# Kernel tuning notes

Hardware: AMD Instinct MI355X
Metric: run time of the kernel (lower is better)

Reference implementation:

```python
import jax, jax.numpy as jnp
import numpy as np


def log_g(x):
    # log of g(x) = x + 0.5 for x>=0, sigmoid(x) for x<0
    return jnp.where(x >= 0, jnp.log(jax.nn.relu(x) + 0.5), -jax.nn.softplus(-x))


def setup_inputs() -> dict:
    key = jax.random.key(0)
    k1, k2, k3 = jax.random.split(key, 3)
    bs, seq_len, d_in, H = 4, 4096, 1024, 1024
    scale = 1.0 / np.sqrt(d_in)  # keep pre-activations O(1) so exp() in log-space scan stays finite
    x = jax.random.normal(k1, (bs, seq_len, d_in), dtype=jnp.float32)
    h_0 = jnp.zeros((bs, 1, H), dtype=jnp.float32)
    Wz = jax.random.normal(k2, (H, d_in), dtype=jnp.float32) * scale
    bz = jnp.zeros((H,), dtype=jnp.float32)
    Wh = jax.random.normal(k3, (H, d_in), dtype=jnp.float32) * scale
    bh = jnp.zeros((H,), dtype=jnp.float32)
    return {"x": x, "h_0": h_0, "Wz": Wz, "bz": bz, "Wh": Wh, "bh": bh}


def reference(x, h_0, Wz, bz, Wh, bh):
    bs, seq_len, _ = x.shape
    # gate and candidate pre-activations (two GEMMs)
    k = jnp.einsum("bsd,hd->bsh", x, Wz) + bz          # [bs, S, H]
    log_coeff = -jax.nn.softplus(k)                     # log(1 - z)
    log_z = -jax.nn.softplus(-k)                        # log(z)
    log_tilde_h = log_g(jnp.einsum("bsd,hd->bsh", x, Wh) + bh)
    log_h_0 = log_g(h_0)                                # [bs, 1, H]
    log_value = jnp.concatenate([log_h_0, log_z + log_tilde_h], axis=1)  # [bs, S+1, H]
    # log-space parallel scan: h_t = (1-z_t) h_{t-1} + z_t h~_t
    a_star = jnp.pad(jnp.cumsum(log_coeff, axis=1), ((0, 0), (1, 0), (0, 0)))  # [bs, S+1, H]
    log_h0_plus_b_star = jax.lax.cumlogsumexp(log_value - a_star, axis=1)
    log_prefix = a_star + log_h0_plus_b_star
    return jnp.exp(log_prefix)[:, 1:]                   # [bs, S, H]
```

## Files before the change

### kernel.cpp

```cpp
#include <hip/hip_runtime.h>
#include <cstddef>
#include <cstdint>

#define BSZ   4
#define SEQ   4096
#define DIN   1024
#define HDIM  1024
#define MTOT  (BSZ * SEQ)
#define NELE  ((size_t)MTOT * HDIM)
#define NX    ((size_t)MTOT * DIN)
#define NW    ((size_t)HDIM * DIN)
#define NCH   128
#define CL    (SEQ / NCH)

#define X4 (NX / 4)
#define W4 (NW / 4)

#define GBM 256
#define GBN 128
#define GBK 64
#define NKT (DIN / GBK)

using bf16x8 = __attribute__((ext_vector_type(8))) __bf16;
using f32x4  = __attribute__((ext_vector_type(4))) float;

__device__ __forceinline__ float bf2f(unsigned int u16bits) {
    union { unsigned int i; float f; } v;
    v.i = u16bits << 16;
    return v.f;
}
__device__ __forceinline__ unsigned int pk2(float a, float b) {
    union { float f; unsigned int i; } ua, ub; ua.f = a; ub.f = b;
    return ((ua.i + 0x8000u) >> 16) | ((ub.i + 0x8000u) & 0xffff0000u);
}

__device__ __forceinline__ void gload16(const void* g, void* l) {
    __builtin_amdgcn_global_load_lds(
        (const __attribute__((address_space(1))) unsigned int*)g,
        (__attribute__((address_space(3))) unsigned int*)l, 16, 0, 0);
}

__global__ __launch_bounds__(256) void cvt_bf16(
    const float* __restrict__ x, const float* __restrict__ wz,
    const float* __restrict__ wh, unsigned short* __restrict__ xb,
    unsigned short* __restrict__ zb, unsigned short* __restrict__ hb)
{
    const size_t i = (size_t)blockIdx.x * 256 + threadIdx.x;
    const float4* s; uint4* d; size_t off;
    const size_t xh = X4 / 2, wh4 = W4 / 2;
    if (i < xh)            { s = (const float4*)x;  d = (uint4*)xb; off = i; }
    else if (i < xh + wh4) { s = (const float4*)wz; d = (uint4*)zb; off = i - xh; }
    else                   { s = (const float4*)wh; d = (uint4*)hb; off = i - xh - wh4; }
    const float4 v0 = s[2 * off];
    const float4 v1 = s[2 * off + 1];
    uint4 r;
    r.x = pk2(v0.x, v0.y); r.y = pk2(v0.z, v0.w);
    r.z = pk2(v1.x, v1.y); r.w = pk2(v1.z, v1.w);
    d[off] = r;
}

#define SBAR  __builtin_amdgcn_sched_barrier(0)
#define PRIO1 __builtin_amdgcn_s_setprio(1)
#define PRIO0 __builtin_amdgcn_s_setprio(0)

#define MFMA1(acc, va, vb) \
    acc = __builtin_amdgcn_mfma_f32_16x16x32_bf16(va, vb, acc, 0, 0, 0)

#define MFMA_PAIR(P, AV, S)                                                    \
    _Pragma("unroll")                                                          \
    for (int i_ = 0; i_ < 2; ++i_) {                                           \
        _Pragma("unroll")                                                      \
        for (int nt_ = 0; nt_ < 2; ++nt_) {                                    \
            MFMA1(accz[2*(P)+i_][nt_], AV[i_][0], Bz[S][nt_][0]);              \
            MFMA1(acch[2*(P)+i_][nt_], AV[i_][0], Bh[S][nt_][0]);              \
            MFMA1(accz[2*(P)+i_][nt_], AV[i_][1], Bz[S][nt_][1]);              \
            MFMA1(acch[2*(P)+i_][nt_], AV[i_][1], Bh[S][nt_][1]);              \
        }                                                                      \
    }

#define READ_A(AV, MTP, B)                                                     \
    AV[0][0] = *(const bf16x8*)((B) + aBase + (2*(MTP)+0)*2048 + k0o);         \
    AV[0][1] = *(const bf16x8*)((B) + aBase + (2*(MTP)+0)*2048 + k1o);         \
    AV[1][0] = *(const bf16x8*)((B) + aBase + (2*(MTP)+1)*2048 + k0o);         \
    AV[1][1] = *(const bf16x8*)((B) + aBase + (2*(MTP)+1)*2048 + k1o);

#define READ_B_HALF(SS, NT, B)                                                 \
    Bz[SS][NT][0] = *(const bf16x8*)((B) + zBase + (NT)*2048 + k0o);           \
    Bz[SS][NT][1] = *(const bf16x8*)((B) + zBase + (NT)*2048 + k1o);           \
    Bh[SS][NT][0] = *(const bf16x8*)((B) + hBase + (NT)*2048 + k0o);           \
    Bh[SS][NT][1] = *(const bf16x8*)((B) + hBase + (NT)*2048 + k1o);

#define STAGE8(BN, KO)                                                         \
    gload16(gA + (KO),          (BN) + ldsA);                                  \
    gload16(gA + (KO) + 16384,  (BN) + ldsA + 512);                            \
    gload16(gA + (KO) + 32768,  (BN) + ldsA + 1024);                           \
    gload16(gA + (KO) + 49152,  (BN) + ldsA + 1536);                           \
    gload16(gZ + (KO),          (BN) + ldsZ);                                  \
    gload16(gZ + (KO) + 16384,  (BN) + ldsZ + 512);                            \
    gload16(gH + (KO),          (BN) + ldsH);                                  \
    gload16(gH + (KO) + 16384,  (BN) + ldsH + 512);

#define TILE(KT, S)                                                            \
    {                                                                          \
        const int ktv = (KT);                                                  \
        const char*     bcc = (const char*)&smem[S][0];                        \
        unsigned short* bn  = &smem[(S) ^ 1][0];                               \
        const char*     bnc = (const char*)bn;                                 \
        const bool pf = (ktv + 1 < NKT);                                       \
        const size_t ko = (size_t)(ktv + 1) * 128;                             \
                                                                       \
        if (pf) { STAGE8(bn, ko) }                                             \
        READ_A(A1, 1, bcc)                                                     \
        PRIO1; MFMA_PAIR(0, A0, S) PRIO0; SBAR;                                \
                                                                       \
        READ_A(A0, 2, bcc)                                                     \
        PRIO1; MFMA_PAIR(1, A1, S) PRIO0; SBAR;                                \
                                                                       \
        READ_A(A1, 3, bcc)                                                     \
        PRIO1; MFMA_PAIR(2, A0, S) PRIO0; SBAR;                                \
                \
        if (pf) {                                                              \
            asm volatile("s_waitcnt vmcnt(0)" ::: "memory");                   \
            __builtin_amdgcn_s_barrier();                                      \
            READ_B_HALF((S) ^ 1, 0, bnc)                                       \
            READ_A(A0, 0, bnc)                                                 \
        }                                                                      \
        PRIO1; MFMA_PAIR(3, A1, S) PRIO0; SBAR;                                \
        if (pf) { READ_B_HALF((S) ^ 1, 1, bnc) }                               \
    }

__global__ __launch_bounds__(512, 2) void gemm_act_8ph(
    const unsigned short* __restrict__ xb, const unsigned short* __restrict__ zb,
    const unsigned short* __restrict__ hb, const float* __restrict__ bz,
    const float* __restrict__ bh, unsigned int* __restrict__ ab,
    float* __restrict__ carryA, float* __restrict__ carryB)
{
    __shared__ unsigned short smem[2][32768];

    const int tid  = threadIdx.x;
    const int wid  = tid >> 6;
    const int lane = tid & 63;
    const int lm   = lane & 15;
    const int q    = lane >> 4;
    const int wr   = wid >> 2;
    const int wc   = wid & 3;

    const int bid = blockIdx.x;
    const int swz = (bid & 7) * 64 + (bid >> 3);
    const int ty  = swz >> 3;
    const int tx  = swz & 7;
    const int m0  = ty * GBM;
    const int n0  = tx * GBN;

    const int l8   = lane >> 3;
    const int sl   = lane & 7;
    const int scol = 16 * (sl ^ l8);
    const char* gA = (const char*)xb + ((size_t)(m0 + wid * 32 + l8) * DIN) * 2 + scol;
    const char* gZ = (const char*)zb + ((size_t)(n0 + wid * 16 + l8) * DIN) * 2 + scol;
    const char* gH = (const char*)hb + ((size_t)(n0 + wid * 16 + l8) * DIN) * 2 + scol;
    const int ldsA = wid * 2048;
    const int ldsZ = 16384 + wid * 1024;
    const int ldsH = 24576 + wid * 1024;

    const int sw  = (lm & 7) << 4;
    const int k0o = (q * 16) ^ sw;
    const int k1o = (64 + q * 16) ^ sw;
    const int aBase = (wr * 128 + lm) * 128;
    const int zBase = 32768 + (wc * 32 + lm) * 128;
    const int hBase = 49152 + (wc * 32 + lm) * 128;

    f32x4 accz[8][2], acch[8][2];
#pragma unroll
    for (int mt = 0; mt < 8; ++mt)
#pragma unroll
        for (int nt = 0; nt < 2; ++nt) {
            accz[mt][nt] = (f32x4){0.f, 0.f, 0.f, 0.f};
            acch[mt][nt] = (f32x4){0.f, 0.f, 0.f, 0.f};
        }

    bf16x8 A0[2][2], A1[2][2];
    bf16x8 Bz[2][2][2], Bh[2][2][2];

    {
        unsigned short* b0 = &smem[0][0];
        const char*     b0c = (const char*)b0;
        STAGE8(b0, 0)
        asm volatile("s_waitcnt vmcnt(0)" ::: "memory");
        __builtin_amdgcn_s_barrier();
        READ_B_HALF(0, 0, b0c)
        READ_B_HALF(0, 1, b0c)
        READ_A(A0, 0, b0c)
    }

    for (int kt = 0; kt < NKT; kt += 2) {
        TILE(kt, 0)
        TILE(kt + 1, 1)
    }

    const int bi  = m0 >> 12;
    const int cb0 = ((m0 & 4095) >> 5) + wr * 4;

#pragma unroll
    for (int nt = 0; nt < 2; ++nt) {
        const int col = n0 + wc * 32 + nt * 16 + lm;
        const float bzv = bz[col];
        const float bhv = bh[col];
#pragma unroll
        for (int pr = 0; pr < 4; ++pr) {
            float CA = 1.f, CB = 0.f;
#pragma unroll
            for (int mi = 0; mi < 2; ++mi) {
                const int mt   = pr * 2 + mi;
                const int row0 = m0 + wr * 128 + mt * 16 + q * 4;
                float A = 1.f, B = 0.f;
#pragma unroll
                for (int r = 0; r < 4; ++r) {
                    const float kpre = accz[mt][nt][r] + bzv;
                    const float hpre = acch[mt][nt][r] + bhv;
                    const float ez   = __expf(-kpre);
                    const float zv   = 1.0f / (1.0f + ez);
                    const float avv  = ez * zv;
                    const float g    = (hpre >= 0.f) ? (hpre + 0.5f)
                                                     : (1.0f / (1.0f + __expf(-hpre)));
                    const float bv   = zv * g;
                    ab[(size_t)(row0 + r) * HDIM + col] = pk2(avv, bv);
                    A = avv * A;
                    B = fmaf(avv, B, bv);
                }
                float A2 = __shfl_xor(A, 16, 64);
                float B2 = __shfl_xor(B, 16, 64);
                B = (q & 1) ? fmaf(A, B2, B) : fmaf(A2, B, B2);
                A = A * A2;
                A2 = __shfl_xor(A, 32, 64);
                B2 = __shfl_xor(B, 32, 64);
                B = (q & 2) ? fmaf(A, B2, B) : fmaf(A2, B, B2);
                A = A * A2;
                CB = fmaf(A, CB, B);
                CA = A * CA;
            }
            if (q == 0) {
                const int cseq = cb0 + pr;
                const size_t ci = ((size_t)(cseq * BSZ + bi)) * HDIM + col;
                carryA[ci] = CA;
                carryB[ci] = CB;
            }
        }
    }
}

__global__ __launch_bounds__(256) void scan_phaseB(
    const float* __restrict__ h0, const float* __restrict__ carryA,
    const float* __restrict__ carryB, float* __restrict__ hin)
{
    const int h  = blockIdx.x * 256 + threadIdx.x;
    const int bi = blockIdx.y;
    const float v = h0[(size_t)bi * HDIM + h];
    float hr = (v >= 0.0f) ? (v + 0.5f) : (1.0f / (1.0f + __expf(-v)));
    for (int c = 0; c < NCH; ++c) {
        const size_t ci = ((size_t)c * BSZ + bi) * HDIM + h;
        hin[ci] = hr;
        hr = fmaf(carryA[ci], hr, carryB[ci]);
    }
}

__global__ __launch_bounds__(256) void scan_phaseC(
    const unsigned int* __restrict__ ab, const float* __restrict__ hin,
    float* __restrict__ out)
{
    const int c  = blockIdx.x;
    const int bi = blockIdx.y;
    const int h  = threadIdx.x * 4;
    size_t idx = ((size_t)bi * SEQ + (size_t)c * CL) * HDIM + h;
    const size_t ci = ((size_t)c * BSZ + bi) * HDIM + h;
    float4 hr = *(const float4*)&hin[ci];
#pragma unroll 4
    for (int t = 0; t < CL; ++t) {
        const uint4 v = *(const uint4*)&ab[idx];
        hr.x = fmaf(bf2f(v.x & 0xffffu), hr.x, bf2f(v.x >> 16));
        hr.y = fmaf(bf2f(v.y & 0xffffu), hr.y, bf2f(v.y >> 16));
        hr.z = fmaf(bf2f(v.z & 0xffffu), hr.z, bf2f(v.z >> 16));
        hr.w = fmaf(bf2f(v.w & 0xffffu), hr.w, bf2f(v.w >> 16));
        *(float4*)&out[idx] = hr;
        idx += HDIM;
    }
}

extern "C" void kernel_launch(void* const* d_in, const int* in_sizes, int n_in,
                              void* d_out, int out_size, void* d_ws, size_t ws_size,
                              hipStream_t stream)
{
    const float* x  = (const float*)d_in[0];
    const float* h0 = (const float*)d_in[1];
    const float* Wz = (const float*)d_in[2];
    const float* bz = (const float*)d_in[3];
    const float* Wh = (const float*)d_in[4];
    const float* bh = (const float*)d_in[5];
    float* out = (float*)d_out;

    unsigned int*   ab  = (unsigned int*)d_ws;
    unsigned short* xbf = (unsigned short*)(ab + NELE);
    unsigned short* zbf = xbf + NX;
    unsigned short* hbf = zbf + NW;
    float* carryA = (float*)(hbf + NW);
    float* carryB = carryA + (size_t)NCH * BSZ * HDIM;
    float* hin    = carryB + (size_t)NCH * BSZ * HDIM;

    const int cvtBlocks = (int)((X4 + 2 * W4) / 2 / 256);
    cvt_bf16<<<cvtBlocks, 256, 0, stream>>>(x, Wz, Wh, xbf, zbf, hbf);

    dim3 gGrid((MTOT / GBM) * (HDIM / GBN));
    gemm_act_8ph<<<gGrid, 512, 0, stream>>>(xbf, zbf, hbf, bz, bh, ab, carryA, carryB);

    dim3 bGrid(HDIM / 256, BSZ);
    scan_phaseB<<<bGrid, 256, 0, stream>>>(h0, carryA, carryB, hin);

    dim3 cGrid(NCH, BSZ);
    scan_phaseC<<<cGrid, 256, 0, stream>>>(ab, hin, out);
}
```

Baseline: 240.1 us.

## Deepen GEMM LDS pipeline to four stages with half-size K tiles

The fused dual GEMM now uses a K tile of 32 instead of 64, spread over a four-slot LDS ring with prefetch distance two, replacing the double buffer. The LDS swizzle and fragment addressing are reworked for 64-byte rows, and the wait on outstanding loads is relaxed to vmcnt(4) so one stage can stay in flight. The goal is to hide global-to-LDS latency better behind the MFMAs, at the cost of twice as many barriers per K pass. Separately, the sequential carry scan in phase B batches eight carry loads ahead of the dependent FMA chain.

```diff
diff --git a/kernel.cpp b/kernel.cpp
--- a/kernel.cpp
+++ b/kernel.cpp
@@ -18,8 +18,8 @@
 
 #define GBM 256
 #define GBN 128
-#define GBK 64
-#define NKT (DIN / GBK)
+#define GBK 32
+#define NKT2 (DIN / GBK)
 
 using bf16x8 = __attribute__((ext_vector_type(8))) __bf16;
 using f32x4  = __attribute__((ext_vector_type(4))) float;
@@ -66,67 +66,55 @@
 #define MFMA1(acc, va, vb) \
     acc = __builtin_amdgcn_mfma_f32_16x16x32_bf16(va, vb, acc, 0, 0, 0)
 
-#define MFMA_PAIR(P, AV, S)                                                    \
+#define MFMA_PH(PH, AV, S)                                                     \
     _Pragma("unroll")                                                          \
-    for (int i_ = 0; i_ < 2; ++i_) {                                           \
+    for (int j_ = 0; j_ < 4; ++j_) {                                           \
         _Pragma("unroll")                                                      \
         for (int nt_ = 0; nt_ < 2; ++nt_) {                                    \
-            MFMA1(accz[2*(P)+i_][nt_], AV[i_][0], Bz[S][nt_][0]);              \
-            MFMA1(acch[2*(P)+i_][nt_], AV[i_][0], Bh[S][nt_][0]);              \
-            MFMA1(accz[2*(P)+i_][nt_], AV[i_][1], Bz[S][nt_][1]);              \
-            MFMA1(acch[2*(P)+i_][nt_], AV[i_][1], Bh[S][nt_][1]);              \
+            MFMA1(accz[4*(PH)+j_][nt_], AV[j_], Bz[S][nt_]);                   \
+            MFMA1(acch[4*(PH)+j_][nt_], AV[j_], Bh[S][nt_]);                   \
         }                                                                      \
     }
 
-#define READ_A(AV, MTP, B)                                                     \
-    AV[0][0] = *(const bf16x8*)((B) + aBase + (2*(MTP)+0)*2048 + k0o);         \
-    AV[0][1] = *(const bf16x8*)((B) + aBase + (2*(MTP)+0)*2048 + k1o);         \
-    AV[1][0] = *(const bf16x8*)((B) + aBase + (2*(MTP)+1)*2048 + k0o);         \
-    AV[1][1] = *(const bf16x8*)((B) + aBase + (2*(MTP)+1)*2048 + k1o);
-
-#define READ_B_HALF(SS, NT, B)                                                 \
-    Bz[SS][NT][0] = *(const bf16x8*)((B) + zBase + (NT)*2048 + k0o);           \
-    Bz[SS][NT][1] = *(const bf16x8*)((B) + zBase + (NT)*2048 + k1o);           \
-    Bh[SS][NT][0] = *(const bf16x8*)((B) + hBase + (NT)*2048 + k0o);           \
-    Bh[SS][NT][1] = *(const bf16x8*)((B) + hBase + (NT)*2048 + k1o);
-
-#define STAGE8(BN, KO)                                                         \
+#define READ_A4(AV, MT0, B)                                                    \
+    AV[0] = *(const bf16x8*)((B) + aBase + ((MT0)+0)*1024);                    \
+    AV[1] = *(const bf16x8*)((B) + aBase + ((MT0)+1)*1024);                    \
+    AV[2] = *(const bf16x8*)((B) + aBase + ((MT0)+2)*1024);                    \
+    AV[3] = *(const bf16x8*)((B) + aBase + ((MT0)+3)*1024);
+
+#define READ_B2(SS, B)                                                         \
+    Bz[SS][0] = *(const bf16x8*)((B) + zBase);                                 \
+    Bh[SS][0] = *(const bf16x8*)((B) + hBase);
+#define READ_B2b(SS, B)                                                        \
+    Bz[SS][1] = *(const bf16x8*)((B) + zBase + 1024);                          \
+    Bh[SS][1] = *(const bf16x8*)((B) + hBase + 1024);
+
+#define STAGE4(BN, KO)                                                         \
     gload16(gA + (KO),          (BN) + ldsA);                                  \
-    gload16(gA + (KO) + 16384,  (BN) + ldsA + 512);                            \
     gload16(gA + (KO) + 32768,  (BN) + ldsA + 1024);                           \
-    gload16(gA + (KO) + 49152,  (BN) + ldsA + 1536);                           \
     gload16(gZ + (KO),          (BN) + ldsZ);                                  \
-    gload16(gZ + (KO) + 16384,  (BN) + ldsZ + 512);                            \
-    gload16(gH + (KO),          (BN) + ldsH);                                  \
-    gload16(gH + (KO) + 16384,  (BN) + ldsH + 512);
+    gload16(gH + (KO),          (BN) + ldsH);
 
 #define TILE(KT, S)                                                            \
     {                                                                          \
         const int ktv = (KT);                                                  \
-        const char*     bcc = (const char*)&smem[S][0];                        \
-        unsigned short* bn  = &smem[(S) ^ 1][0];                               \
-        const char*     bnc = (const char*)bn;                                 \
-        const bool pf = (ktv + 1 < NKT);                                       \
-        const size_t ko = (size_t)(ktv + 1) * 128;                             \
-                                                                       \
-        if (pf) { STAGE8(bn, ko) }                                             \
-        READ_A(A1, 1, bcc)                                                     \
-        PRIO1; MFMA_PAIR(0, A0, S) PRIO0; SBAR;                                \
-                                                                       \
-        READ_A(A0, 2, bcc)                                                     \
-        PRIO1; MFMA_PAIR(1, A1, S) PRIO0; SBAR;                                \
-                                                                       \
-        READ_A(A1, 3, bcc)                                                     \
-        PRIO1; MFMA_PAIR(2, A0, S) PRIO0; SBAR;                                \
-                \
-        if (pf) {                                                              \
-            asm volatile("s_waitcnt vmcnt(0)" ::: "memory");                   \
+        const char* bcc = (const char*)smem[(S)];                              \
+        const char* bnx = (const char*)smem[((S)+1)&3];                        \
+        char*       bs2 = smem[((S)+2)&3];                                     \
+                                \
+        if (ktv + 2 < NKT2) { STAGE4(bs2, (size_t)(ktv+2)*64) }                \
+        READ_A4(A1, 4, bcc)                                                    \
+        PRIO1; MFMA_PH(0, A0, (S)&1) PRIO0; SBAR;                              \
+               \
+        if (ktv + 1 < NKT2) {                                                  \
+            if (ktv >= NKT2 - 2) { asm volatile("s_waitcnt vmcnt(0)" ::: "memory"); } \
+            else                 { asm volatile("s_waitcnt vmcnt(4)" ::: "memory"); } \
             __builtin_amdgcn_s_barrier();                                      \
-            READ_B_HALF((S) ^ 1, 0, bnc)                                       \
-            READ_A(A0, 0, bnc)                                                 \
+            READ_B2((((S)+1)&1), bnx)                                          \
+            READ_A4(A0, 0, bnx)                                                \
         }                                                                      \
-        PRIO1; MFMA_PAIR(3, A1, S) PRIO0; SBAR;                                \
-        if (pf) { READ_B_HALF((S) ^ 1, 1, bnc) }                               \
+        PRIO1; MFMA_PH(1, A1, (S)&1) PRIO0; SBAR;                              \
+        if (ktv + 1 < NKT2) { READ_B2b((((S)+1)&1), bnx) }                     \
     }
 
 __global__ __launch_bounds__(512, 2) void gemm_act_8ph(
@@ -135,7 +123,7 @@
     const float* __restrict__ bh, unsigned int* __restrict__ ab,
     float* __restrict__ carryA, float* __restrict__ carryB)
 {
-    __shared__ unsigned short smem[2][32768];
+    __shared__ char smem[4][32768];
 
     const int tid  = threadIdx.x;
     const int wid  = tid >> 6;
@@ -152,22 +140,20 @@
     const int m0  = ty * GBM;
     const int n0  = tx * GBN;
 
-    const int l8   = lane >> 3;
-    const int sl   = lane & 7;
-    const int scol = 16 * (sl ^ l8);
-    const char* gA = (const char*)xb + ((size_t)(m0 + wid * 32 + l8) * DIN) * 2 + scol;
-    const char* gZ = (const char*)zb + ((size_t)(n0 + wid * 16 + l8) * DIN) * 2 + scol;
-    const char* gH = (const char*)hb + ((size_t)(n0 + wid * 16 + l8) * DIN) * 2 + scol;
+    const int l16  = lane >> 2;
+    const int xs   = ((lane >> 2) & 3) ^ ((lane >> 4) & 3);
+    const int scol = ((lane & 3) ^ xs) << 4;
+    const char* gA = (const char*)xb + ((size_t)(m0 + wid * 32 + l16) * DIN) * 2 + scol;
+    const char* gZ = (const char*)zb + ((size_t)(n0 + wid * 16 + l16) * DIN) * 2 + scol;
+    const char* gH = (const char*)hb + ((size_t)(n0 + wid * 16 + l16) * DIN) * 2 + scol;
     const int ldsA = wid * 2048;
     const int ldsZ = 16384 + wid * 1024;
     const int ldsH = 24576 + wid * 1024;
 
-    const int sw  = (lm & 7) << 4;
-    const int k0o = (q * 16) ^ sw;
-    const int k1o = (64 + q * 16) ^ sw;
-    const int aBase = (wr * 128 + lm) * 128;
-    const int zBase = 32768 + (wc * 32 + lm) * 128;
-    const int hBase = 49152 + (wc * 32 + lm) * 128;
+    const int kxo  = ((q ^ (lm & 3) ^ ((lm >> 2) & 3)) << 4);
+    const int aBase = (wr * 128 + lm) * 64 + kxo;
+    const int zBase = 16384 + (wc * 32 + lm) * 64 + kxo;
+    const int hBase = 24576 + (wc * 32 + lm) * 64 + kxo;
 
     f32x4 accz[8][2], acch[8][2];
 #pragma unroll
@@ -178,23 +164,27 @@
             acch[mt][nt] = (f32x4){0.f, 0.f, 0.f, 0.f};
         }
 
-    bf16x8 A0[2][2], A1[2][2];
-    bf16x8 Bz[2][2][2], Bh[2][2][2];
+    bf16x8 A0[4], A1[4];
+    bf16x8 Bz[2][2], Bh[2][2];
 
     {
-        unsigned short* b0 = &smem[0][0];
-        const char*     b0c = (const char*)b0;
-        STAGE8(b0, 0)
-        asm volatile("s_waitcnt vmcnt(0)" ::: "memory");
+        char* b0 = smem[0];
+        char* b1 = smem[1];
+        STAGE4(b0, 0)
+        STAGE4(b1, 64)
+        asm volatile("s_waitcnt vmcnt(4)" ::: "memory");
         __builtin_amdgcn_s_barrier();
-        READ_B_HALF(0, 0, b0c)
-        READ_B_HALF(0, 1, b0c)
-        READ_A(A0, 0, b0c)
-    }
-
-    for (int kt = 0; kt < NKT; kt += 2) {
-        TILE(kt, 0)
+        const char* b0c = (const char*)b0;
+        READ_B2(0, b0c)
+        READ_B2b(0, b0c)
+        READ_A4(A0, 0, b0c)
+    }
+
+    for (int kt = 0; kt < NKT2; kt += 4) {
+        TILE(kt,     0)
         TILE(kt + 1, 1)
+        TILE(kt + 2, 2)
+        TILE(kt + 3, 3)
     }
 
     const int bi  = m0 >> 12;
@@ -256,10 +246,20 @@
     const int bi = blockIdx.y;
     const float v = h0[(size_t)bi * HDIM + h];
     float hr = (v >= 0.0f) ? (v + 0.5f) : (1.0f / (1.0f + __expf(-v)));
-    for (int c = 0; c < NCH; ++c) {
-        const size_t ci = ((size_t)c * BSZ + bi) * HDIM + h;
-        hin[ci] = hr;
-        hr = fmaf(carryA[ci], hr, carryB[ci]);
+    for (int c0 = 0; c0 < NCH; c0 += 8) {
+        float a[8], b[8];
+#pragma unroll
+        for (int j = 0; j < 8; ++j) {
+            const size_t ci = ((size_t)(c0 + j) * BSZ + bi) * HDIM + h;
+            a[j] = carryA[ci];
+            b[j] = carryB[ci];
+        }
+#pragma unroll
+        for (int j = 0; j < 8; ++j) {
+            const size_t ci = ((size_t)(c0 + j) * BSZ + bi) * HDIM + h;
+            hin[ci] = hr;
+            hr = fmaf(a[j], hr, b[j]);
+        }
     }
 }
 
```

Measured after the change: 285.4 us. 18.8% more time.

## Deepen GEMM prefetch to two tiles ahead and batch carry loads in scan

Applied to the files above, without the earlier changes.

The GEMM main loop now issues global-to-LDS loads two k-tiles ahead into the buffer just consumed, waiting with vmcnt(8) so one tile's loads stay in flight across the barrier. To make the in-place overwrite safe it adds an lgkmcnt wait and an extra barrier, and the launch bound changes from 2 to 1 blocks per SM, which may loosen register limits but lowers occupancy. Separately, the phase-B carry scan now loads eight carryA/carryB values at once before running the serial recurrence, hiding memory latency in that loop.

```diff
diff --git a/kernel.cpp b/kernel.cpp
--- a/kernel.cpp
+++ b/kernel.cpp
@@ -104,23 +104,27 @@
     {                                                                          \
         const int ktv = (KT);                                                  \
         const char*     bcc = (const char*)&smem[S][0];                        \
-        unsigned short* bn  = &smem[(S) ^ 1][0];                               \
-        const char*     bnc = (const char*)bn;                                 \
+        unsigned short* bcw = &smem[S][0];                                     \
+        const char*     bnc = (const char*)&smem[(S) ^ 1][0];                  \
         const bool pf = (ktv + 1 < NKT);                                       \
-        const size_t ko = (size_t)(ktv + 1) * 128;                             \
+        const size_t ko2 = (size_t)(ktv + 2) * 128;                            \
                                                                        \
-        if (pf) { STAGE8(bn, ko) }                                             \
         READ_A(A1, 1, bcc)                                                     \
         PRIO1; MFMA_PAIR(0, A0, S) PRIO0; SBAR;                                \
                                                                        \
         READ_A(A0, 2, bcc)                                                     \
         PRIO1; MFMA_PAIR(1, A1, S) PRIO0; SBAR;                                \
-                                                                       \
+              \
         READ_A(A1, 3, bcc)                                                     \
+        asm volatile("s_waitcnt lgkmcnt(0)" ::: "memory");                     \
+        SBAR;                                                                  \
+        __builtin_amdgcn_s_barrier();                                          \
+        if (ktv + 2 < NKT) { STAGE8(bcw, ko2) }                                \
         PRIO1; MFMA_PAIR(2, A0, S) PRIO0; SBAR;                                \
-                \
+         \
         if (pf) {                                                              \
-            asm volatile("s_waitcnt vmcnt(0)" ::: "memory");                   \
+            if (ktv + 2 < NKT) { asm volatile("s_waitcnt vmcnt(8)" ::: "memory"); } \
+            else               { asm volatile("s_waitcnt vmcnt(0)" ::: "memory"); } \
             __builtin_amdgcn_s_barrier();                                      \
             READ_B_HALF((S) ^ 1, 0, bnc)                                       \
             READ_A(A0, 0, bnc)                                                 \
@@ -129,7 +133,7 @@
         if (pf) { READ_B_HALF((S) ^ 1, 1, bnc) }                               \
     }
 
-__global__ __launch_bounds__(512, 2) void gemm_act_8ph(
+__global__ __launch_bounds__(512, 1) void gemm_act_8ph(
     const unsigned short* __restrict__ xb, const unsigned short* __restrict__ zb,
     const unsigned short* __restrict__ hb, const float* __restrict__ bz,
     const float* __restrict__ bh, unsigned int* __restrict__ ab,
@@ -183,9 +187,11 @@
 
     {
         unsigned short* b0 = &smem[0][0];
+        unsigned short* b1 = &smem[1][0];
         const char*     b0c = (const char*)b0;
         STAGE8(b0, 0)
-        asm volatile("s_waitcnt vmcnt(0)" ::: "memory");
+        STAGE8(b1, 128)
+        asm volatile("s_waitcnt vmcnt(8)" ::: "memory");
         __builtin_amdgcn_s_barrier();
         READ_B_HALF(0, 0, b0c)
         READ_B_HALF(0, 1, b0c)
@@ -256,10 +262,20 @@
     const int bi = blockIdx.y;
     const float v = h0[(size_t)bi * HDIM + h];
     float hr = (v >= 0.0f) ? (v + 0.5f) : (1.0f / (1.0f + __expf(-v)));
-    for (int c = 0; c < NCH; ++c) {
-        const size_t ci = ((size_t)c * BSZ + bi) * HDIM + h;
-        hin[ci] = hr;
-        hr = fmaf(carryA[ci], hr, carryB[ci]);
+    for (int c0 = 0; c0 < NCH; c0 += 8) {
+        float a[8], b[8];
+#pragma unroll
+        for (int j = 0; j < 8; ++j) {
+            const size_t ci = ((size_t)(c0 + j) * BSZ + bi) * HDIM + h;
+            a[j] = carryA[ci];
+            b[j] = carryB[ci];
+        }
+#pragma unroll
+        for (int j = 0; j < 8; ++j) {
+            const size_t ci = ((size_t)(c0 + j) * BSZ + bi) * HDIM + h;
+            hin[ci] = hr;
+            hr = fmaf(a[j], hr, b[j]);
+        }
     }
 }
 
```

Result: no change. 241.3 us (+0.5%).

## Make GEMM blocks persistent over two M-tiles and double scan chunk count

Applied to the files above, without the earlier changes.

The GEMM grid is halved so each block processes two M tiles in sequence. The first K tile of the second rep is prefetched during the last tile of the first, and launch bounds drop to one block per CU. Scan chunks go from 128 to 256, so chunk carries are written per 16-row MFMA tile instead of combined pairs, shortening the sequential phase C loop. Phase B batches its carry loads into registers, MFMA issue order is reshuffled by k-half, and phase C unroll is raised. The cost is lower occupancy and a longer serial chain in phase B.

```diff
diff --git a/kernel.cpp b/kernel.cpp
--- a/kernel.cpp
+++ b/kernel.cpp
@@ -10,7 +10,7 @@
 #define NELE  ((size_t)MTOT * HDIM)
 #define NX    ((size_t)MTOT * DIN)
 #define NW    ((size_t)HDIM * DIN)
-#define NCH   128
+#define NCH   256
 #define CL    (SEQ / NCH)
 
 #define X4 (NX / 4)
@@ -20,6 +20,7 @@
 #define GBN 128
 #define GBK 64
 #define NKT (DIN / GBK)
+#define AOFF ((size_t)8192 * 2048)
 
 using bf16x8 = __attribute__((ext_vector_type(8))) __bf16;
 using f32x4  = __attribute__((ext_vector_type(4))) float;
@@ -68,13 +69,14 @@
 
 #define MFMA_PAIR(P, AV, S)                                                    \
     _Pragma("unroll")                                                          \
-    for (int i_ = 0; i_ < 2; ++i_) {                                           \
+    for (int kk_ = 0; kk_ < 2; ++kk_) {                                        \
         _Pragma("unroll")                                                      \
-        for (int nt_ = 0; nt_ < 2; ++nt_) {                                    \
-            MFMA1(accz[2*(P)+i_][nt_], AV[i_][0], Bz[S][nt_][0]);              \
-            MFMA1(acch[2*(P)+i_][nt_], AV[i_][0], Bh[S][nt_][0]);              \
-            MFMA1(accz[2*(P)+i_][nt_], AV[i_][1], Bz[S][nt_][1]);              \
-            MFMA1(acch[2*(P)+i_][nt_], AV[i_][1], Bh[S][nt_][1]);              \
+        for (int i_ = 0; i_ < 2; ++i_) {                                       \
+            _Pragma("unroll")                                                  \
+            for (int nt_ = 0; nt_ < 2; ++nt_) {                                \
+                MFMA1(accz[2*(P)+i_][nt_], AV[i_][kk_], Bz[S][nt_][kk_]);      \
+                MFMA1(acch[2*(P)+i_][nt_], AV[i_][kk_], Bh[S][nt_][kk_]);      \
+            }                                                                  \
         }                                                                      \
     }
 
@@ -90,15 +92,15 @@
     Bh[SS][NT][0] = *(const bf16x8*)((B) + hBase + (NT)*2048 + k0o);           \
     Bh[SS][NT][1] = *(const bf16x8*)((B) + hBase + (NT)*2048 + k1o);
 
-#define STAGE8(BN, KO)                                                         \
-    gload16(gA + (KO),          (BN) + ldsA);                                  \
-    gload16(gA + (KO) + 16384,  (BN) + ldsA + 512);                            \
-    gload16(gA + (KO) + 32768,  (BN) + ldsA + 1024);                           \
-    gload16(gA + (KO) + 49152,  (BN) + ldsA + 1536);                           \
-    gload16(gZ + (KO),          (BN) + ldsZ);                                  \
-    gload16(gZ + (KO) + 16384,  (BN) + ldsZ + 512);                            \
-    gload16(gH + (KO),          (BN) + ldsH);                                  \
-    gload16(gH + (KO) + 16384,  (BN) + ldsH + 512);
+#define STAGE8(PA, BN, KO)                                                     \
+    gload16((PA) + (KO),          (BN) + ldsA);                                \
+    gload16((PA) + (KO) + 16384,  (BN) + ldsA + 512);                          \
+    gload16((PA) + (KO) + 32768,  (BN) + ldsA + 1024);                         \
+    gload16((PA) + (KO) + 49152,  (BN) + ldsA + 1536);                         \
+    gload16(gZ + (KO),            (BN) + ldsZ);                                \
+    gload16(gZ + (KO) + 16384,    (BN) + ldsZ + 512);                          \
+    gload16(gH + (KO),            (BN) + ldsH);                                \
+    gload16(gH + (KO) + 16384,    (BN) + ldsH + 512);
 
 #define TILE(KT, S)                                                            \
     {                                                                          \
@@ -109,7 +111,7 @@
         const bool pf = (ktv + 1 < NKT);                                       \
         const size_t ko = (size_t)(ktv + 1) * 128;                             \
                                                                        \
-        if (pf) { STAGE8(bn, ko) }                                             \
+        if (pf) { STAGE8(gAr, bn, ko) }                                        \
         READ_A(A1, 1, bcc)                                                     \
         PRIO1; MFMA_PAIR(0, A0, S) PRIO0; SBAR;                                \
                                                                        \
@@ -118,7 +120,7 @@
                                                                        \
         READ_A(A1, 3, bcc)                                                     \
         PRIO1; MFMA_PAIR(2, A0, S) PRIO0; SBAR;                                \
-                \
+                                                                       \
         if (pf) {                                                              \
             asm volatile("s_waitcnt vmcnt(0)" ::: "memory");                   \
             __builtin_amdgcn_s_barrier();                                      \
@@ -129,7 +131,20 @@
         if (pf) { READ_B_HALF((S) ^ 1, 1, bnc) }                               \
     }
 
-__global__ __launch_bounds__(512, 2) void gemm_act_8ph(
+#define TILE15(FIRSTREP)                                                       \
+    {                                                                          \
+        const char* bcc = (const char*)&smem[1][0];                            \
+        READ_A(A1, 1, bcc)                                                     \
+        if (FIRSTREP) { STAGE8(gAr + AOFF, &smem[0][0], 0) }                   \
+        PRIO1; MFMA_PAIR(0, A0, 1) PRIO0; SBAR;                                \
+        READ_A(A0, 2, bcc)                                                     \
+        PRIO1; MFMA_PAIR(1, A1, 1) PRIO0; SBAR;                                \
+        READ_A(A1, 3, bcc)                                                     \
+        PRIO1; MFMA_PAIR(2, A0, 1) PRIO0; SBAR;                                \
+        PRIO1; MFMA_PAIR(3, A1, 1) PRIO0; SBAR;                                \
+    }
+
+__global__ __launch_bounds__(512, 1) void gemm_act_8ph(
     const unsigned short* __restrict__ xb, const unsigned short* __restrict__ zb,
     const unsigned short* __restrict__ hb, const float* __restrict__ bz,
     const float* __restrict__ bh, unsigned int* __restrict__ ab,
@@ -146,10 +161,10 @@
     const int wc   = wid & 3;
 
     const int bid = blockIdx.x;
-    const int swz = (bid & 7) * 64 + (bid >> 3);
-    const int ty  = swz >> 3;
-    const int tx  = swz & 7;
-    const int m0  = ty * GBM;
+    const int s   = (bid & 7) * 32 + (bid >> 3);
+    const int tx  = s & 7;
+    const int typ = s >> 3;
+    const int m0  = typ * GBM;
     const int n0  = tx * GBN;
 
     const int l8   = lane >> 3;
@@ -158,6 +173,7 @@
     const char* gA = (const char*)xb + ((size_t)(m0 + wid * 32 + l8) * DIN) * 2 + scol;
     const char* gZ = (const char*)zb + ((size_t)(n0 + wid * 16 + l8) * DIN) * 2 + scol;
     const char* gH = (const char*)hb + ((size_t)(n0 + wid * 16 + l8) * DIN) * 2 + scol;
+    const char* gAr = gA;
     const int ldsA = wid * 2048;
     const int ldsZ = 16384 + wid * 1024;
     const int ldsH = 24576 + wid * 1024;
@@ -170,48 +186,48 @@
     const int hBase = 49152 + (wc * 32 + lm) * 128;
 
     f32x4 accz[8][2], acch[8][2];
-#pragma unroll
-    for (int mt = 0; mt < 8; ++mt)
-#pragma unroll
-        for (int nt = 0; nt < 2; ++nt) {
-            accz[mt][nt] = (f32x4){0.f, 0.f, 0.f, 0.f};
-            acch[mt][nt] = (f32x4){0.f, 0.f, 0.f, 0.f};
-        }
-
     bf16x8 A0[2][2], A1[2][2];
     bf16x8 Bz[2][2][2], Bh[2][2][2];
 
     {
-        unsigned short* b0 = &smem[0][0];
-        const char*     b0c = (const char*)b0;
-        STAGE8(b0, 0)
+        STAGE8(gAr, &smem[0][0], 0)
         asm volatile("s_waitcnt vmcnt(0)" ::: "memory");
         __builtin_amdgcn_s_barrier();
+    }
+
+#pragma unroll 1
+    for (int rep = 0; rep < 2; ++rep) {
+        const char* b0c = (const char*)&smem[0][0];
+#pragma unroll
+        for (int mt = 0; mt < 8; ++mt)
+#pragma unroll
+            for (int nt = 0; nt < 2; ++nt) {
+                accz[mt][nt] = (f32x4){0.f, 0.f, 0.f, 0.f};
+                acch[mt][nt] = (f32x4){0.f, 0.f, 0.f, 0.f};
+            }
         READ_B_HALF(0, 0, b0c)
         READ_B_HALF(0, 1, b0c)
         READ_A(A0, 0, b0c)
-    }
-
-    for (int kt = 0; kt < NKT; kt += 2) {
-        TILE(kt, 0)
-        TILE(kt + 1, 1)
-    }
-
-    const int bi  = m0 >> 12;
-    const int cb0 = ((m0 & 4095) >> 5) + wr * 4;
-
-#pragma unroll
-    for (int nt = 0; nt < 2; ++nt) {
-        const int col = n0 + wc * 32 + nt * 16 + lm;
-        const float bzv = bz[col];
-        const float bhv = bh[col];
-#pragma unroll
-        for (int pr = 0; pr < 4; ++pr) {
-            float CA = 1.f, CB = 0.f;
-#pragma unroll
-            for (int mi = 0; mi < 2; ++mi) {
-                const int mt   = pr * 2 + mi;
-                const int row0 = m0 + wr * 128 + mt * 16 + q * 4;
+
+        for (int kt = 0; kt < 14; kt += 2) {
+            TILE(kt, 0)
+            TILE(kt + 1, 1)
+        }
+        TILE(14, 0)
+        TILE15(rep == 0)
+
+        const int m0r = m0 + rep * 8192;
+        const int bi  = m0r >> 12;
+        const int cb0 = ((m0r & 4095) >> 4) + wr * 8;
+
+#pragma unroll
+        for (int nt = 0; nt < 2; ++nt) {
+            const int col = n0 + wc * 32 + nt * 16 + lm;
+            const float bzv = bz[col];
+            const float bhv = bh[col];
+#pragma unroll
+            for (int mt = 0; mt < 8; ++mt) {
+                const int row0 = m0r + wr * 128 + mt * 16 + q * 4;
                 float A = 1.f, B = 0.f;
 #pragma unroll
                 for (int r = 0; r < 4; ++r) {
@@ -235,15 +251,19 @@
                 B2 = __shfl_xor(B, 32, 64);
                 B = (q & 2) ? fmaf(A, B2, B) : fmaf(A2, B, B2);
                 A = A * A2;
-                CB = fmaf(A, CB, B);
-                CA = A * CA;
+                if (q == 0) {
+                    const int cseq = cb0 + mt;
+                    const size_t ci = ((size_t)(cseq * BSZ + bi)) * HDIM + col;
+                    carryA[ci] = A;
+                    carryB[ci] = B;
+                }
             }
-            if (q == 0) {
-                const int cseq = cb0 + pr;
-                const size_t ci = ((size_t)(cseq * BSZ + bi)) * HDIM + col;
-                carryA[ci] = CA;
-                carryB[ci] = CB;
-            }
+        }
+
+        if (rep == 0) {
+            asm volatile("s_waitcnt vmcnt(0)" ::: "memory");
+            __builtin_amdgcn_s_barrier();
+            gAr += AOFF;
         }
     }
 }
@@ -256,10 +276,20 @@
     const int bi = blockIdx.y;
     const float v = h0[(size_t)bi * HDIM + h];
     float hr = (v >= 0.0f) ? (v + 0.5f) : (1.0f / (1.0f + __expf(-v)));
-    for (int c = 0; c < NCH; ++c) {
-        const size_t ci = ((size_t)c * BSZ + bi) * HDIM + h;
-        hin[ci] = hr;
-        hr = fmaf(carryA[ci], hr, carryB[ci]);
+    for (int c0 = 0; c0 < NCH; c0 += 32) {
+        float a[32], b[32];
+#pragma unroll
+        for (int j = 0; j < 32; ++j) {
+            const size_t ci = ((size_t)(c0 + j) * BSZ + bi) * HDIM + h;
+            a[j] = carryA[ci];
+            b[j] = carryB[ci];
+        }
+#pragma unroll
+        for (int j = 0; j < 32; ++j) {
+            const size_t ci = ((size_t)(c0 + j) * BSZ + bi) * HDIM + h;
+            hin[ci] = hr;
+            hr = fmaf(a[j], hr, b[j]);
+        }
     }
 }
 
@@ -273,7 +303,7 @@
     size_t idx = ((size_t)bi * SEQ + (size_t)c * CL) * HDIM + h;
     const size_t ci = ((size_t)c * BSZ + bi) * HDIM + h;
     float4 hr = *(const float4*)&hin[ci];
-#pragma unroll 4
+#pragma unroll 8
     for (int t = 0; t < CL; ++t) {
         const uint4 v = *(const uint4*)&ab[idx];
         hr.x = fmaf(bf2f(v.x & 0xffffu), hr.x, bf2f(v.x >> 16));
@@ -308,7 +338,7 @@
     const int cvtBlocks = (int)((X4 + 2 * W4) / 2 / 256);
     cvt_bf16<<<cvtBlocks, 256, 0, stream>>>(x, Wz, Wh, xbf, zbf, hbf);
 
-    dim3 gGrid((MTOT / GBM) * (HDIM / GBN));
+    dim3 gGrid((MTOT / GBM / 2) * (HDIM / GBN));
     gemm_act_8ph<<<gGrid, 512, 0, stream>>>(xbf, zbf, hbf, bz, bh, ab, carryA, carryB);
 
     dim3 bGrid(HDIM / 256, BSZ);
```

Result: slower. 261.0 us (+8.7%).
